# Kernel optimization log

Hardware: AMD Instinct MI355X
Metric: run time of the kernel (lower is better)

## Reference

```python
import jax, jax.numpy as jnp
import numpy as np

D_MODEL = 1024
STATE_DIM = 128


def setup_inputs() -> dict:
    key = jax.random.key(0)
    ks = jax.random.split(key, 8)
    B, T, D, N = 8, 4096, D_MODEL, STATE_DIM
    u = jax.random.normal(ks[0], (B, T, D), dtype=jnp.float32)
    h0 = jnp.zeros((B, N), dtype=jnp.float32)
    log_A = jax.random.normal(ks[1], (N,), dtype=jnp.float32) * 0.1 - 1.0
    B_w = jax.random.normal(ks[2], (N, D), dtype=jnp.float32) / np.sqrt(D)
    B_b = jax.random.normal(ks[3], (N,), dtype=jnp.float32) * 0.01
    C_w = jax.random.normal(ks[4], (D, N), dtype=jnp.float32) / np.sqrt(N)
    C_b = jax.random.normal(ks[5], (D,), dtype=jnp.float32) * 0.01
    D_param = jnp.ones((D,), dtype=jnp.float32) * 0.1
    log_dt = jax.random.normal(ks[6], (N,), dtype=jnp.float32) * 0.1 - 2.0
    return {"u": u, "h0": h0, "log_A": log_A, "B_w": B_w, "B_b": B_b,
            "C_w": C_w, "C_b": C_b, "D_param": D_param, "log_dt": log_dt}


def reference(u, h0, log_A, B_w, B_b, C_w, C_b, D_param, log_dt):
    # u: [B, T, D], h0: [B, N]
    dt = jnp.minimum(jnp.exp(log_dt), 1.0)          # [N]
    A = -jnp.exp(log_A)                             # [N]
    A_bar = jnp.exp(A * dt)                         # [N]
    # B_bar * u, precomputed for all timesteps: [B, T, N]
    Bu = (jnp.einsum('btd,nd->btn', u, B_w) + B_b) * dt

    def step(h, bu_t):
        h = A_bar * h + bu_t                        # [B, N]
        return h, h

    # scan over time: Bu transposed to [T, B, N]
    _, hs = jax.lax.scan(step, h0, jnp.swapaxes(Bu, 0, 1))
    hs = jnp.swapaxes(hs, 0, 1)                     # [B, T, N]
    # y = C h + c_bias + D * u
    y = jnp.einsum('btn,dn->btd', hs, C_w) + C_b + D_param * u
    return y
```

## Files before the change

kernel.cpp:

```cpp
#include <hip/hip_runtime.h>

#define B_SZ 8
#define T_SZ 4096
#define D_SZ 1024
#define N_SZ 128
#define M_SZ (B_SZ*T_SZ)
#define C1 32
#define NC1 (T_SZ/C1)
#define C2 64
#define NC2 (T_SZ/C2)

typedef __attribute__((ext_vector_type(8))) __bf16 bf16x8;
typedef __attribute__((ext_vector_type(4))) float f32x4;
typedef __attribute__((ext_vector_type(4))) unsigned int u32x4;
typedef __attribute__((ext_vector_type(4))) float fvec4;

static __device__ __forceinline__ unsigned short f2bf(float f){
  union { float f; unsigned int u; } v; v.f = f;
  unsigned int r = v.u + 0x7fffu + ((v.u >> 16) & 1u);
  return (unsigned short)(r >> 16);
}

static __device__ __forceinline__ float bf2f(unsigned short s){
  union { unsigned int u; float f; } v; v.u = ((unsigned)s) << 16;
  return v.f;
}

static __device__ __forceinline__ void cp16(const void* g, void* l){
  __builtin_amdgcn_global_load_lds(
      (const __attribute__((address_space(1))) void*)g,
      (__attribute__((address_space(3))) void*)l, 16, 0, 0);
}

static __device__ __forceinline__ f32x4 zero4(){
  f32x4 v = {0.f, 0.f, 0.f, 0.f};
  return v;
}

static __device__ __forceinline__ bf16x8 pack8(fvec4 a, fvec4 b){
  bf16x8 v;
  v[0]=(__bf16)a.x; v[1]=(__bf16)a.y; v[2]=(__bf16)a.z; v[3]=(__bf16)a.w;
  v[4]=(__bf16)b.x; v[5]=(__bf16)b.y; v[6]=(__bf16)b.z; v[7]=(__bf16)b.w;
  return v;
}

__global__ __launch_bounds__(256) void k_conv(const float* __restrict__ Bw,
                                              const float* __restrict__ Cw,
                                              unsigned short* __restrict__ bw,
                                              unsigned short* __restrict__ cw){
  int t = blockIdx.x*256 + threadIdx.x;
  {
    int n = t >> 10, k = t & 1023;
    int c = k >> 6, kk = k & 63;
    unsigned byte = (unsigned)c*16384u + (unsigned)n*128u
                  + (unsigned)((kk*2) ^ ((n&7)<<4));
    bw[byte>>1] = f2bf(Bw[n*1024 + k]);
  }
  {
    int d = t >> 7, k = t & 127;
    int c = d >> 7, dd = d & 127;
    unsigned byte = (unsigned)c*32768u + (unsigned)dd*256u
                  + (unsigned)((k*2) ^ ((dd&15)<<4));
    cw[byte>>1] = f2bf(Cw[d*128 + k]);
  }
}

__global__ __launch_bounds__(256, 4) void k_gemm1c(const float* __restrict__ u,
                                                   const unsigned short* __restrict__ bw,
                                                   const float* __restrict__ Bb,
                                                   const float* __restrict__ logA,
                                                   const float* __restrict__ logdt,
                                                   unsigned short* __restrict__ Bu_bf,
                                                   float* __restrict__ carry){
  __shared__ __align__(16) char smem[20480];
  unsigned short* lA = (unsigned short*)smem;
  unsigned short* lB = (unsigned short*)(smem + 4096);
  float*          BuT = (float*)smem;
  const int tid  = threadIdx.x;
  const int lane = tid & 63;
  const int wave = tid >> 6;
  const int bc   = blockIdx.x;
  const int m0   = bc * 32;
  const int l15  = lane & 15;
  const int lhi  = lane >> 4;
  const int rt   = (wave & 1) * 16;
  const int ct0  = (wave >> 1) * 4;

  f32x4 acc[4];
  #pragma unroll
  for (int i=0;i<4;++i) acc[i] = zero4();

  for (int kc=0; kc<16; ++kc){
    #pragma unroll
    for (int rep=0; rep<4; ++rep){
      const char* g = (const char*)bw + kc*16384 + rep*4096 + tid*16;
      cp16(g, (char*)lB + rep*4096 + tid*16);
    }
    {
      int row = tid >> 3, ks = tid & 7;
      const float* src = u + (size_t)(m0+row)*1024 + kc*64 + ks*8;
      fvec4 f0 = *(const fvec4*)src;
      fvec4 f1 = *(const fvec4*)(src+4);
      unsigned byte = (unsigned)row*128u + (unsigned)((ks*16) ^ ((row&7)<<4));
      *(bf16x8*)((char*)lA + byte) = pack8(f0, f1);
    }
    __syncthreads();
    #pragma unroll
    for (int k0=0; k0<64; k0+=32){
      int arow = rt + l15;
      int ak = k0 + lhi*8;
      bf16x8 af = *(const bf16x8*)((const char*)lA + arow*128 + ((ak*2) ^ ((arow&7)<<4)));
      #pragma unroll
      for (int j=0;j<4;++j){
        int bn = (ct0+j)*16 + l15;
        bf16x8 bfv = *(const bf16x8*)((const char*)lB + bn*128 + ((ak*2) ^ ((bn&7)<<4)));
        acc[j] = __builtin_amdgcn_mfma_f32_16x16x32_bf16(af, bfv, acc[j], 0, 0, 0);
      }
    }
    __syncthreads();
  }

  #pragma unroll
  for (int j=0;j<4;++j){
    int n = (ct0+j)*16 + l15;
    float dt = fminf(__expf(logdt[n]), 1.f);
    float bb = Bb[n];
    #pragma unroll
    for (int r=0;r<4;++r){
      int ml = rt + lhi*4 + r;
      BuT[ml*128 + n] = (acc[j][r] + bb) * dt;
    }
  }
  __syncthreads();

  #pragma unroll
  for (int i=0;i<2;++i){
    int q = i*256 + tid;
    const float* s = BuT + q*8;
    fvec4 a = *(const fvec4*)s;
    fvec4 b = *(const fvec4*)(s+4);
    u32x4 p;
    p.x = (unsigned)f2bf(a.x) | ((unsigned)f2bf(a.y)<<16);
    p.y = (unsigned)f2bf(a.z) | ((unsigned)f2bf(a.w)<<16);
    p.z = (unsigned)f2bf(b.x) | ((unsigned)f2bf(b.y)<<16);
    p.w = (unsigned)f2bf(b.z) | ((unsigned)f2bf(b.w)<<16);
    *(u32x4*)((char*)Bu_bf + (size_t)bc*8192 + (size_t)q*16) = p;
  }

  if (tid < 128){
    int n = tid;
    float dt = fminf(__expf(logdt[n]), 1.f);
    float Ab = __expf(-__expf(logA[n]) * dt);
    float h = 0.f;
    #pragma unroll 8
    for (int j=0;j<C1;++j) h = fmaf(Ab, h, BuT[j*128 + n]);
    carry[(size_t)bc*128 + n] = h;
  }
}

__global__ __launch_bounds__(256) void k_gemm2s(const unsigned short* __restrict__ Bu_bf,
                                                const float* __restrict__ carry,
                                                const unsigned short* __restrict__ cw,
                                                const float* __restrict__ u,
                                                const float* __restrict__ h0,
                                                const float* __restrict__ Cb,
                                                const float* __restrict__ Dp,
                                                const float* __restrict__ logA,
                                                const float* __restrict__ logdt,
                                                float* __restrict__ y){
  __shared__ __align__(16) unsigned short BuT[64*128];
  __shared__ __align__(16) unsigned short hsT[64*128];
  __shared__ __align__(16) unsigned short cwT[128*128];
  const int tid = threadIdx.x, lane = tid & 63, wave = tid >> 6;
  const int bc = blockIdx.x;
  const int m0 = bc * 64;
  const int l15 = lane & 15, lhi = lane >> 4;

  #pragma unroll
  for (int i=0;i<4;++i){
    int off = i*4096 + tid*16;
    cp16((const char*)Bu_bf + (size_t)bc*16384 + off, (char*)BuT + off);
  }
  #pragma unroll
  for (int i=0;i<8;++i){
    int off = i*4096 + tid*16;
    cp16((const char*)cw + off, (char*)cwT + off);
  }

  float hreg = 0.f, Ab = 0.f;
  if (tid < 128){
    int n = tid;
    int b = bc >> 6;
    int c32 = (bc & 63) * 2;
    float dt = fminf(__expf(logdt[n]), 1.f);
    float Ad = -__expf(logA[n]) * dt;
    Ab = __expf(Ad);
    float AL = __expf(Ad * (float)C1);
    float h = h0[b*128 + n];
    const float* cp = carry + (size_t)b*NC1*128 + n;
    for (int g=0; g<8; ++g){
      if (g*16 >= c32) break;
      float cbuf[16];
      #pragma unroll
      for (int i=0;i<16;++i) cbuf[i] = cp[(size_t)(g*16+i)*128];
      #pragma unroll
      for (int i=0;i<16;++i){
        int idx = g*16 + i;
        h = (idx < c32) ? fmaf(AL, h, cbuf[i]) : h;
      }
    }
    hreg = h;
  }
  __syncthreads();

  if (tid < 128){
    int n = tid;
    float h = hreg;
    #pragma unroll 8
    for (int j=0;j<C2;++j){
      h = fmaf(Ab, h, bf2f(BuT[j*128 + n]));
      unsigned byte = (unsigned)j*256u + (unsigned)((n*2) ^ ((j&15)<<4));
      *(unsigned short*)((char*)hsT + byte) = f2bf(h);
    }
  }
  __syncthreads();

  for (int d=0; d<8; ++d){
    f32x4 acc[8];
    #pragma unroll
    for (int i=0;i<8;++i) acc[i] = zero4();

    #pragma unroll
    for (int k0=0;k0<128;k0+=32){
      int arow = wave*16 + l15;
      int ak = k0 + lhi*8;
      bf16x8 af = *(const bf16x8*)((const char*)hsT + arow*256 + ((ak*2) ^ ((arow&15)<<4)));
      #pragma unroll
      for (int ct=0;ct<8;++ct){
        int dn = ct*16 + l15;
        bf16x8 bfv = *(const bf16x8*)((const char*)cwT + dn*256 + ((ak*2) ^ ((dn&15)<<4)));
        acc[ct] = __builtin_amdgcn_mfma_f32_16x16x32_bf16(af, bfv, acc[ct], 0, 0, 0);
      }
    }
    __syncthreads();

    if (d < 7){
      #pragma unroll
      for (int i=0;i<8;++i){
        int off = (wave*8 + i)*1024 + lane*16;
        cp16((const char*)cw + (size_t)(d+1)*32768 + off, (char*)cwT + off);
      }
    }

    const int d0 = d*128;
    #pragma unroll
    for (int ct=0;ct<8;++ct){
      int dc = d0 + ct*16 + l15;
      float cb = Cb[dc], dp = Dp[dc];
      #pragma unroll
      for (int r=0;r<4;++r){
        int m = m0 + wave*16 + lhi*4 + r;
        size_t off = (size_t)m*1024 + dc;
        y[off] = acc[ct][r] + cb + dp*u[off];
      }
    }
    __syncthreads();
  }
}

extern "C" void kernel_launch(void* const* d_in, const int* in_sizes, int n_in,
                              void* d_out, int out_size, void* d_ws, size_t ws_size,
                              hipStream_t stream){
  (void)in_sizes; (void)n_in; (void)out_size; (void)ws_size;
  const float* u     = (const float*)d_in[0];
  const float* h0    = (const float*)d_in[1];
  const float* logA  = (const float*)d_in[2];
  const float* Bw    = (const float*)d_in[3];
  const float* Bb    = (const float*)d_in[4];
  const float* Cw    = (const float*)d_in[5];
  const float* Cb    = (const float*)d_in[6];
  const float* Dp    = (const float*)d_in[7];
  const float* logdt = (const float*)d_in[8];
  float* y = (float*)d_out;

  char* ws = (char*)d_ws;
  unsigned short* Bu_bf = (unsigned short*)(ws);
  float*          carry = (float*)(ws + 8388608);
  unsigned short* bw    = (unsigned short*)(ws + 8912896);
  unsigned short* cw    = (unsigned short*)(ws + 9175040);

  k_conv  <<<dim3(512),  dim3(256), 0, stream>>>(Bw, Cw, bw, cw);
  k_gemm1c<<<dim3(1024), dim3(256), 0, stream>>>(u, bw, Bb, logA, logdt, Bu_bf, carry);
  k_gemm2s<<<dim3(512),  dim3(256), 0, stream>>>(Bu_bf, carry, cw, u, h0, Cb, Dp,
                                                 logA, logdt, y);
}
```

Before: 85.45 us.

## Halve gemm2 row tile to 32 and double grid for more blocks

The second GEMM kernel now handles 32 time rows per block instead of 64 and launches 1024 blocks. Its four waves are split as two row tiles by two column halves. The staged Bu tile in shared memory is dropped: the scan reads Bu directly from global memory, which also removes one barrier. The aim is more parallelism and occupancy (launch bounds 256,4, smaller LDS footprint) on a 256-CU part. In exchange, each block reloads the full C weight tile for only half the rows, which doubles weight traffic, and the serial carry prefix loop now runs over up to 127 chunks per block.

```diff
diff --git a/kernel.cpp b/kernel.cpp
--- a/kernel.cpp
+++ b/kernel.cpp
@@ -7,8 +7,6 @@
 #define M_SZ (B_SZ*T_SZ)
 #define C1 32
 #define NC1 (T_SZ/C1)
-#define C2 64
-#define NC2 (T_SZ/C2)
 
 typedef __attribute__((ext_vector_type(8))) __bf16 bf16x8;
 typedef __attribute__((ext_vector_type(4))) float f32x4;
@@ -158,7 +156,8 @@
   }
 }
 
-__global__ __launch_bounds__(256) void k_gemm2s(const unsigned short* __restrict__ Bu_bf,
+__global__ __launch_bounds__(256, 4) void k_gemm2s(
+                                                const unsigned short* __restrict__ Bu_bf,
                                                 const float* __restrict__ carry,
                                                 const unsigned short* __restrict__ cw,
                                                 const float* __restrict__ u,
@@ -168,19 +167,15 @@
                                                 const float* __restrict__ logA,
                                                 const float* __restrict__ logdt,
                                                 float* __restrict__ y){
-  __shared__ __align__(16) unsigned short BuT[64*128];
-  __shared__ __align__(16) unsigned short hsT[64*128];
+  __shared__ __align__(16) unsigned short hsT[32*128];
   __shared__ __align__(16) unsigned short cwT[128*128];
   const int tid = threadIdx.x, lane = tid & 63, wave = tid >> 6;
   const int bc = blockIdx.x;
-  const int m0 = bc * 64;
+  const int m0 = bc * 32;
   const int l15 = lane & 15, lhi = lane >> 4;
-
-  #pragma unroll
-  for (int i=0;i<4;++i){
-    int off = i*4096 + tid*16;
-    cp16((const char*)Bu_bf + (size_t)bc*16384 + off, (char*)BuT + off);
-  }
+  const int mt  = wave & 1;
+  const int ct0 = (wave >> 1) * 4;
+
   #pragma unroll
   for (int i=0;i<8;++i){
     int off = i*4096 + tid*16;
@@ -190,8 +185,8 @@
   float hreg = 0.f, Ab = 0.f;
   if (tid < 128){
     int n = tid;
-    int b = bc >> 6;
-    int c32 = (bc & 63) * 2;
+    int b = bc >> 7;
+    int c32 = bc & 127;
     float dt = fminf(__expf(logdt[n]), 1.f);
     float Ad = -__expf(logA[n]) * dt;
     Ab = __expf(Ad);
@@ -211,14 +206,14 @@
     }
     hreg = h;
   }
-  __syncthreads();
 
   if (tid < 128){
     int n = tid;
     float h = hreg;
+    const unsigned short* bp = Bu_bf + (size_t)bc*4096 + n;
     #pragma unroll 8
-    for (int j=0;j<C2;++j){
-      h = fmaf(Ab, h, bf2f(BuT[j*128 + n]));
+    for (int j=0;j<C1;++j){
+      h = fmaf(Ab, h, bf2f(bp[(size_t)j*128]));
       unsigned byte = (unsigned)j*256u + (unsigned)((n*2) ^ ((j&15)<<4));
       *(unsigned short*)((char*)hsT + byte) = f2bf(h);
     }
@@ -226,20 +221,20 @@
   __syncthreads();
 
   for (int d=0; d<8; ++d){
-    f32x4 acc[8];
-    #pragma unroll
-    for (int i=0;i<8;++i) acc[i] = zero4();
+    f32x4 acc[4];
+    #pragma unroll
+    for (int i=0;i<4;++i) acc[i] = zero4();
 
     #pragma unroll
     for (int k0=0;k0<128;k0+=32){
-      int arow = wave*16 + l15;
+      int arow = mt*16 + l15;
       int ak = k0 + lhi*8;
       bf16x8 af = *(const bf16x8*)((const char*)hsT + arow*256 + ((ak*2) ^ ((arow&15)<<4)));
       #pragma unroll
-      for (int ct=0;ct<8;++ct){
-        int dn = ct*16 + l15;
+      for (int j=0;j<4;++j){
+        int dn = (ct0+j)*16 + l15;
         bf16x8 bfv = *(const bf16x8*)((const char*)cwT + dn*256 + ((ak*2) ^ ((dn&15)<<4)));
-        acc[ct] = __builtin_amdgcn_mfma_f32_16x16x32_bf16(af, bfv, acc[ct], 0, 0, 0);
+        acc[j] = __builtin_amdgcn_mfma_f32_16x16x32_bf16(af, bfv, acc[j], 0, 0, 0);
       }
     }
     __syncthreads();
@@ -254,14 +249,14 @@
 
     const int d0 = d*128;
     #pragma unroll
-    for (int ct=0;ct<8;++ct){
-      int dc = d0 + ct*16 + l15;
+    for (int j=0;j<4;++j){
+      int dc = d0 + (ct0+j)*16 + l15;
       float cb = Cb[dc], dp = Dp[dc];
       #pragma unroll
       for (int r=0;r<4;++r){
-        int m = m0 + wave*16 + lhi*4 + r;
+        int m = m0 + mt*16 + lhi*4 + r;
         size_t off = (size_t)m*1024 + dc;
-        y[off] = acc[ct][r] + cb + dp*u[off];
+        y[off] = acc[j][r] + cb + dp*u[off];
       }
     }
     __syncthreads();
@@ -291,6 +286,6 @@
 
   k_conv  <<<dim3(512),  dim3(256), 0, stream>>>(Bw, Cw, bw, cw);
   k_gemm1c<<<dim3(1024), dim3(256), 0, stream>>>(u, bw, Bb, logA, logdt, Bu_bf, carry);
-  k_gemm2s<<<dim3(512),  dim3(256), 0, stream>>>(Bu_bf, carry, cw, u, h0, Cb, Dp,
+  k_gemm2s<<<dim3(1024), dim3(256), 0, stream>>>(Bu_bf, carry, cw, u, h0, Cb, Dp,
                                                  logA, logdt, y);
 }
```

Measured after the change: 105.3 us. 1.23x slower.

## Double gemm2 block to 512 threads and read C weights directly from global

Applied to the files above, without the earlier changes.

The second GEMM kernel now runs 512 threads (8 waves) per block. Each wave owns a 16-column slice of the output and covers all 64 rows, where before each of 4 waves took 16 rows and all 128 columns. The shared-memory copy of the C weight tile and its per-iteration syncthreads are removed; each wave loads its B fragments directly from global/L2 and prefetches u values before the MFMA loop. This cuts LDS use and barriers and raises parallelism, at the cost of redundant global reads of the C weights across blocks and more register pressure.

```diff
diff --git a/kernel.cpp b/kernel.cpp
--- a/kernel.cpp
+++ b/kernel.cpp
@@ -158,7 +158,8 @@
   }
 }
 
-__global__ __launch_bounds__(256) void k_gemm2s(const unsigned short* __restrict__ Bu_bf,
+__global__ __launch_bounds__(512, 2) void k_gemm2s(
+                                                const unsigned short* __restrict__ Bu_bf,
                                                 const float* __restrict__ carry,
                                                 const unsigned short* __restrict__ cw,
                                                 const float* __restrict__ u,
@@ -170,21 +171,15 @@
                                                 float* __restrict__ y){
   __shared__ __align__(16) unsigned short BuT[64*128];
   __shared__ __align__(16) unsigned short hsT[64*128];
-  __shared__ __align__(16) unsigned short cwT[128*128];
   const int tid = threadIdx.x, lane = tid & 63, wave = tid >> 6;
   const int bc = blockIdx.x;
   const int m0 = bc * 64;
   const int l15 = lane & 15, lhi = lane >> 4;
 
   #pragma unroll
-  for (int i=0;i<4;++i){
-    int off = i*4096 + tid*16;
+  for (int i=0;i<2;++i){
+    int off = i*8192 + tid*16;
     cp16((const char*)Bu_bf + (size_t)bc*16384 + off, (char*)BuT + off);
-  }
-  #pragma unroll
-  for (int i=0;i<8;++i){
-    int off = i*4096 + tid*16;
-    cp16((const char*)cw + off, (char*)cwT + off);
   }
 
   float hreg = 0.f, Ab = 0.f;
@@ -225,46 +220,55 @@
   }
   __syncthreads();
 
+  const int dn = wave*16 + l15;
+
   for (int d=0; d<8; ++d){
-    f32x4 acc[8];
-    #pragma unroll
-    for (int i=0;i<8;++i) acc[i] = zero4();
-
-    #pragma unroll
-    for (int k0=0;k0<128;k0+=32){
-      int arow = wave*16 + l15;
-      int ak = k0 + lhi*8;
-      bf16x8 af = *(const bf16x8*)((const char*)hsT + arow*256 + ((ak*2) ^ ((arow&15)<<4)));
-      #pragma unroll
-      for (int ct=0;ct<8;++ct){
-        int dn = ct*16 + l15;
-        bf16x8 bfv = *(const bf16x8*)((const char*)cwT + dn*256 + ((ak*2) ^ ((dn&15)<<4)));
-        acc[ct] = __builtin_amdgcn_mfma_f32_16x16x32_bf16(af, bfv, acc[ct], 0, 0, 0);
-      }
-    }
-    __syncthreads();
-
-    if (d < 7){
-      #pragma unroll
-      for (int i=0;i<8;++i){
-        int off = (wave*8 + i)*1024 + lane*16;
-        cp16((const char*)cw + (size_t)(d+1)*32768 + off, (char*)cwT + off);
-      }
-    }
-
     const int d0 = d*128;
-    #pragma unroll
-    for (int ct=0;ct<8;++ct){
-      int dc = d0 + ct*16 + l15;
-      float cb = Cb[dc], dp = Dp[dc];
+    const char* cwd = (const char*)cw + (size_t)d*32768;
+
+    bf16x8 bf[4];
+    #pragma unroll
+    for (int k0i=0;k0i<4;++k0i){
+      int ak = k0i*32 + lhi*8;
+      bf[k0i] = *(const bf16x8*)(cwd + dn*256 + ((ak*2) ^ ((dn&15)<<4)));
+    }
+
+    const int dc = d0 + dn;
+    float cb = Cb[dc], dp = Dp[dc];
+    float up[4][4];
+    #pragma unroll
+    for (int mt=0;mt<4;++mt){
       #pragma unroll
       for (int r=0;r<4;++r){
-        int m = m0 + wave*16 + lhi*4 + r;
+        int m = m0 + mt*16 + lhi*4 + r;
+        up[mt][r] = u[(size_t)m*1024 + dc];
+      }
+    }
+
+    f32x4 acc[4];
+    #pragma unroll
+    for (int i=0;i<4;++i) acc[i] = zero4();
+
+    #pragma unroll
+    for (int k0i=0;k0i<4;++k0i){
+      int ak = k0i*32 + lhi*8;
+      #pragma unroll
+      for (int mt=0;mt<4;++mt){
+        int arow = mt*16 + l15;
+        bf16x8 af = *(const bf16x8*)((const char*)hsT + arow*256 + ((ak*2) ^ ((arow&15)<<4)));
+        acc[mt] = __builtin_amdgcn_mfma_f32_16x16x32_bf16(af, bf[k0i], acc[mt], 0, 0, 0);
+      }
+    }
+
+    #pragma unroll
+    for (int mt=0;mt<4;++mt){
+      #pragma unroll
+      for (int r=0;r<4;++r){
+        int m = m0 + mt*16 + lhi*4 + r;
         size_t off = (size_t)m*1024 + dc;
-        y[off] = acc[ct][r] + cb + dp*u[off];
-      }
-    }
-    __syncthreads();
+        y[off] = acc[mt][r] + cb + dp*up[mt][r];
+      }
+    }
   }
 }
 
@@ -291,6 +295,6 @@
 
   k_conv  <<<dim3(512),  dim3(256), 0, stream>>>(Bw, Cw, bw, cw);
   k_gemm1c<<<dim3(1024), dim3(256), 0, stream>>>(u, bw, Bb, logA, logdt, Bu_bf, carry);
-  k_gemm2s<<<dim3(512),  dim3(256), 0, stream>>>(Bu_bf, carry, cw, u, h0, Cb, Dp,
+  k_gemm2s<<<dim3(512),  dim3(512), 0, stream>>>(Bu_bf, carry, cw, u, h0, Cb, Dp,
                                                  logA, logdt, y);
 }
```

Result: slower. 89.56 us (+4.8%).
